# Performance work log

Measured on AMD Instinct MI355X. Metric: run time of the kernel, lower is better.

Reference implementation:

```python
import jax, jax.numpy as jnp
import numpy as np

NUM_STEPS = 151
STEP = 2.0 / (NUM_STEPS - 1)
TSIZE = NUM_STEPS  # t = -1, -1+step, ..., 1
N = 4096
D = 512
NUM_CLASSES = 100


def setup_inputs() -> dict:
    key = jax.random.key(0)
    k1, k2 = jax.random.split(key)
    feats = jax.random.normal(k1, (N, D), dtype=jnp.float32)
    # L2-normalize so pairwise dot products lie in [-1, 1] (histogram support)
    feats = feats / jnp.linalg.norm(feats, axis=1, keepdims=True)
    classes = jax.random.randint(k2, (N,), 0, NUM_CLASSES, dtype=jnp.int64)
    return {"features": feats, "classes": classes}


def reference(features, classes):
    n = features.shape[0]
    # pairwise cosine similarities, upper triangle (i < j)
    dists = features @ features.T  # [N, N]
    iu, ju = jnp.triu_indices(n, k=1)  # static index arrays
    s = dists[iu, ju]                  # [P] similarities
    pos = classes[iu] == classes[ju]   # [P] same-class mask

    # triangular soft-binning exactly as in the torch code:
    # f = floor(s/step)*step; bin at t==f gets (s-f)/step, bin at t==f+step gets (f+step-s)/step
    f = jnp.floor(s / STEP) * STEP
    j = jnp.floor(s / STEP).astype(jnp.int32) + (NUM_STEPS - 1) // 2  # index of t == f
    wa = (s - f) / STEP
    wb = (f + STEP - s) / STEP
    va = (j >= 0) & (j < TSIZE)
    vb = (j + 1 >= 0) & (j + 1 < TSIZE)
    ja = jnp.clip(j, 0, TSIZE - 1)
    jb = jnp.clip(j + 1, 0, TSIZE - 1)

    def hist(mask, size):
        w_a = jnp.where(va & mask, wa, 0.0)
        w_b = jnp.where(vb & mask, wb, 0.0)
        h = jnp.zeros(TSIZE, s.dtype).at[ja].add(w_a).at[jb].add(w_b)
        return h / size.astype(s.dtype)

    pos_size = pos.sum()
    neg_size = (~pos).sum()
    hist_pos = hist(pos, pos_size)
    hist_neg = hist(~pos, neg_size)
    # tril-masked repeat + sum(0) == inclusive cumulative sum of hist_pos
    hist_pos_cdf = jnp.cumsum(hist_pos)
    loss = jnp.sum(hist_neg * hist_pos_cdf)
    return loss
```

## Files before the change

### kernel.cpp

```cpp
#include <hip/hip_runtime.h>


#define N_PTS   4096
#define DIM     512
#define TSIZE   151
#define HALF_T  75
#define BM      128
#define BK      64
#define NSTEP   24
#define NTILES  32
#define NBLOCKS 528
#define P_TOTAL 8386560u
#define STEPF   (2.0f / 150.0f)
#define STEPINV 75.0f
#define NCOPY   8
#define HSTRIDE 309

typedef short bfrag __attribute__((ext_vector_type(8)));
typedef float ffrag __attribute__((ext_vector_type(4)));
typedef unsigned short u16;
typedef unsigned int   u32;

__device__ __forceinline__ ffrag mfma16(bfrag a, bfrag b, ffrag c) {
  return __builtin_amdgcn_mfma_f32_16x16x32_bf16(a, b, c, 0, 0, 0);
}

__device__ __forceinline__ void split4(float4 v, uint2* hi, uint2* lo) {
  u32 u0 = __float_as_uint(v.x), u1 = __float_as_uint(v.y);
  u32 u2 = __float_as_uint(v.z), u3 = __float_as_uint(v.w);
  float r0 = v.x - __uint_as_float(u0 & 0xFFFF0000u);
  float r1 = v.y - __uint_as_float(u1 & 0xFFFF0000u);
  float r2 = v.z - __uint_as_float(u2 & 0xFFFF0000u);
  float r3 = v.w - __uint_as_float(u3 & 0xFFFF0000u);
  hi->x = (u0 >> 16) | (u1 & 0xFFFF0000u);
  hi->y = (u2 >> 16) | (u3 & 0xFFFF0000u);
  lo->x = (__float_as_uint(r0) >> 16) | (__float_as_uint(r1) & 0xFFFF0000u);
  lo->y = (__float_as_uint(r2) >> 16) | (__float_as_uint(r3) & 0xFFFF0000u);
}

__device__ __forceinline__ void tile_decode(int orig, int* bi_, int* bj_) {
  int sbid = (orig & 7) * 66 + (orig >> 3);
  int rem = sbid, cnt = NTILES, bi = 0;
  while (rem >= cnt) { rem -= cnt; --cnt; ++bi; }
  *bi_ = bi; *bj_ = bi + rem;
}

__device__ __forceinline__ void stage_step(
    int s, u16* Ad, u16* Bd,
    const u16* __restrict__ Fhi, const u16* __restrict__ Flo,
    int rowA, int rowB, int w, int rseg, int swzk)
{
  const int region = s >> 3;
  const int k0 = (s & 7) * BK;
  const u16* ap = (region == 1) ? Flo : Fhi;
  const u16* bp = (region == 2) ? Flo : Fhi;
  #pragma unroll
  for (int g = 0; g < 4; ++g) {
    int seg = w * 4 + g;
    int row = seg * 8 + rseg;
    size_t ga = (size_t)(rowA + row) * DIM + k0 + swzk;
    size_t gb = (size_t)(rowB + row) * DIM + k0 + swzk;
    __builtin_amdgcn_global_load_lds(
        (const __attribute__((address_space(1))) unsigned int*)(ap + ga),
        (__attribute__((address_space(3))) unsigned int*)(Ad + seg * 512),
        16, 0, 0);
    __builtin_amdgcn_global_load_lds(
        (const __attribute__((address_space(1))) unsigned int*)(bp + gb),
        (__attribute__((address_space(3))) unsigned int*)(Bd + seg * 512),
        16, 0, 0);
  }
}

__device__ __forceinline__ void compute_step(
    const u16* As, const u16* Bs, ffrag (&acc)[4][4],
    int wy, int wx, int l4, int l16)
{
  const int swz = (l16 & 7) << 3;
  #pragma unroll
  for (int ks = 0; ks < 2; ++ks) {
    bfrag a[4], b[4];
    #pragma unroll
    for (int f = 0; f < 4; ++f) {
      int ra = wy * 64 + f * 16 + l16;
      int rb = wx * 64 + f * 16 + l16;
      int ko = (ks * 32 + l4 * 8) ^ swz;
      a[f] = *(const bfrag*)(As + ra * BK + ko);
      b[f] = *(const bfrag*)(Bs + rb * BK + ko);
    }
    #pragma unroll
    for (int fj = 0; fj < 4; ++fj)
      #pragma unroll
      for (int fi = 0; fi < 4; ++fi)
        acc[fi][fj] = mfma16(a[fi], b[fj], acc[fi][fj]);
  }
}

__device__ __forceinline__ void bin_epilogue(
    const ffrag (&acc)[4][4], float* h, const int* clsA, const int* clsB,
    int wy, int wx, int l4, int l16, bool diag, u32* myPos)
{
  #pragma unroll
  for (int fi = 0; fi < 4; ++fi) {
    #pragma unroll
    for (int fj = 0; fj < 4; ++fj) {
      #pragma unroll
      for (int r = 0; r < 4; ++r) {
        int li = wy * 64 + fi * 16 + l4 * 4 + r;
        int lj = wx * 64 + fj * 16 + l16;
        if (diag && li >= lj) continue;
        float s  = acc[fi][fj][r];
        float jf = floorf(s * STEPINV);
        int   jb = (int)jf + HALF_T;
        float f  = jf * STEPF;
        float wa = (s - f) * STEPINV;
        float wb = (f + STEPF - s) * STEPINV;
        bool  pos = (clsA[li] == clsB[lj]);
        *myPos += pos ? 1u : 0u;
        int off = pos ? 0 : TSIZE;
        if (jb >= 0 && jb < TSIZE)         unsafeAtomicAdd(h + off + jb, wa);
        if (jb + 1 >= 0 && jb + 1 < TSIZE) unsafeAtomicAdd(h + off + jb + 1, wb);
      }
    }
  }
}

__global__ __launch_bounds__(256) void presplit(
    const float* __restrict__ F, u16* __restrict__ Fhi, u16* __restrict__ Flo,
    float* __restrict__ g_hist, u32* __restrict__ g_pos)
{
  int u = blockIdx.x * 256 + threadIdx.x;
  int row = u >> 6, kb = u & 63;
  const float* src = F + (size_t)row * DIM + kb * 8;
  float4 v0 = *(const float4*)(src);
  float4 v1 = *(const float4*)(src + 4);
  uint2 h0, l0, h1, l1;
  split4(v0, &h0, &l0);
  split4(v1, &h1, &l1);
  uint4 hv; hv.x = h0.x; hv.y = h0.y; hv.z = h1.x; hv.w = h1.y;
  uint4 lv; lv.x = l0.x; lv.y = l0.y; lv.z = l1.x; lv.w = l1.y;
  size_t dst = (size_t)row * DIM + kb * 8;
  *(uint4*)(Fhi + dst) = hv;
  *(uint4*)(Flo + dst) = lv;
  if (blockIdx.x == 0) {
    for (int i = threadIdx.x; i < 2 * TSIZE; i += 256) g_hist[i] = 0.0f;
    if (threadIdx.x == 0) *g_pos = 0u;
  }
}

__global__ __launch_bounds__(256, 2) void hist_mfma(
    const u16* __restrict__ Fhi, const u16* __restrict__ Flo,
    const int* __restrict__ cls,
    float* __restrict__ g_hist, u32* __restrict__ g_pos)
{
  __shared__ __align__(16) u16 As0[BM * BK];
  __shared__ __align__(16) u16 As1[BM * BK];
  __shared__ __align__(16) u16 Bs0[BM * BK];
  __shared__ __align__(16) u16 Bs1[BM * BK];
  __shared__ float hist[NCOPY * HSTRIDE];
  __shared__ int clsA[BM], clsB[BM];
  __shared__ u32 posCount;

  const int t = threadIdx.x;
  int bi, bj;
  tile_decode((int)blockIdx.x, &bi, &bj);
  const int rowA = bi * BM, rowB = bj * BM;

  for (int i = t; i < NCOPY * HSTRIDE; i += 256) hist[i] = 0.0f;
  if (t < BM) clsA[t] = cls[rowA + t];
  else        clsB[t - BM] = cls[rowB + (t - BM)];
  if (t == 0) posCount = 0u;

  const int lane = t & 63, w = t >> 6;
  const int wy = w >> 1, wx = w & 1;
  const int l4 = lane >> 4, l16 = lane & 15;
  const int rseg = lane >> 3;
  const int swzk = ((lane & 7) ^ (lane >> 3)) << 3;

  ffrag acc[4][4] = {};

  stage_step(0, As0, Bs0, Fhi, Flo, rowA, rowB, w, rseg, swzk);
  __syncthreads();

  #pragma unroll 1
  for (int s2 = 0; s2 < NSTEP / 2; ++s2) {
    const int s = s2 * 2;
    if (s + 1 < NSTEP) stage_step(s + 1, As1, Bs1, Fhi, Flo, rowA, rowB, w, rseg, swzk);
    compute_step(As0, Bs0, acc, wy, wx, l4, l16);
    __syncthreads();
    if (s + 2 < NSTEP) stage_step(s + 2, As0, Bs0, Fhi, Flo, rowA, rowB, w, rseg, swzk);
    compute_step(As1, Bs1, acc, wy, wx, l4, l16);
    __syncthreads();
  }

  u32 myPos = 0;
  float* h = hist + (lane & 7) * HSTRIDE;
  bin_epilogue(acc, h, clsA, clsB, wy, wx, l4, l16, bi == bj, &myPos);
  atomicAdd(&posCount, myPos);
  __syncthreads();

  for (int i = t; i < 2 * TSIZE; i += 256) {
    float v = 0.0f;
    #pragma unroll
    for (int c = 0; c < NCOPY; ++c) v += hist[c * HSTRIDE + i];
    unsafeAtomicAdd(g_hist + i, v);
  }
  if (t == 0) atomicAdd(g_pos, posCount);
}

__global__ __launch_bounds__(256) void finalize(
    const float* __restrict__ g_hist,
    const u32* __restrict__ g_pos,
    float* __restrict__ out)
{
  __shared__ float hp[TSIZE];
  __shared__ float hn[TSIZE];
  __shared__ float red[4];
  const int t = threadIdx.x;
  const float Np = (float)(*g_pos);
  const float Nn = (float)(P_TOTAL - *g_pos);
  if (t < TSIZE) {
    hp[t] = g_hist[t] / Np;
    hn[t] = g_hist[TSIZE + t] / Nn;
  }
  __syncthreads();
  for (int off = 1; off < TSIZE; off <<= 1) {
    float v = 0.0f;
    if (t < TSIZE && t >= off) v = hp[t - off];
    __syncthreads();
    if (t < TSIZE) hp[t] += v;
    __syncthreads();
  }
  float term = (t < TSIZE) ? hn[t] * hp[t] : 0.0f;
  #pragma unroll
  for (int o = 32; o > 0; o >>= 1) term += __shfl_down(term, o);
  if ((t & 63) == 0) red[t >> 6] = term;
  __syncthreads();
  if (t == 0) *out = red[0] + red[1] + red[2] + red[3];
}

extern "C" void kernel_launch(void* const* d_in, const int* in_sizes, int n_in,
                              void* d_out, int out_size, void* d_ws, size_t ws_size,
                              hipStream_t stream) {
  const float* F   = (const float*)d_in[0];
  const int*   cls = (const int*)d_in[1];
  float* g_hist = (float*)d_ws;
  u32*   g_pos  = (u32*)((char*)d_ws + 2 * TSIZE * sizeof(float));
  float* out = (float*)d_out;

  const size_t offH = 65536;
  u16* Fhi = (u16*)((char*)d_ws + offH);
  u16* Flo = (u16*)((char*)d_ws + offH + (size_t)N_PTS * DIM * sizeof(u16));

  presplit<<<(N_PTS * 64) / 256, 256, 0, stream>>>(F, Fhi, Flo, g_hist, g_pos);
  hist_mfma<<<NBLOCKS, 256, 0, stream>>>(Fhi, Flo, cls, g_hist, g_pos);
  finalize<<<1, 256, 0, stream>>>(g_hist, g_pos, out);
}
```

Baseline: 234.5 us.

## Single-buffer LDS for 3 blocks/CU and XCD-aware band tile mapping

```diff
diff --git a/kernel.cpp b/kernel.cpp
--- a/kernel.cpp
+++ b/kernel.cpp
@@ -8,13 +8,12 @@
 #define BM      128
 #define BK      64
 #define NSTEP   24
-#define NTILES  32
-#define NBLOCKS 528
 #define P_TOTAL 8386560u
 #define STEPF   (2.0f / 150.0f)
 #define STEPINV 75.0f
 #define NCOPY   8
 #define HSTRIDE 309
+#define GRID    576
 
 typedef short bfrag __attribute__((ext_vector_type(8)));
 typedef float ffrag __attribute__((ext_vector_type(4)));
@@ -38,11 +37,24 @@
   lo->y = (__float_as_uint(r2) >> 16) | (__float_as_uint(r3) & 0xFFFF0000u);
 }
 
-__device__ __forceinline__ void tile_decode(int orig, int* bi_, int* bj_) {
-  int sbid = (orig & 7) * 66 + (orig >> 3);
-  int rem = sbid, cnt = NTILES, bi = 0;
-  while (rem >= cnt) { rem -= cnt; --cnt; ++bi; }
-  *bi_ = bi; *bj_ = bi + rem;
+__device__ __forceinline__ bool tile_decode(int bid, int* bi_, int* bj_) {
+  const int xcd = bid & 7, slot = bid >> 3;
+  if (xcd < 6) {
+    if (slot >= 64) return false;
+    const int BA[6] = {0, 0, 0, 1, 1, 2};
+    const int BB[6] = {1, 2, 3, 2, 3, 3};
+    *bi_ = BA[xcd] * 8 + (slot >> 3);
+    *bj_ = BB[xcd] * 8 + (slot & 7);
+  } else {
+    int p = slot;
+    int band = (xcd - 6) * 2 + (p >= 36 ? 1 : 0);
+    if (p >= 36) p -= 36;
+    int rem = p, cnt = 8, ii = 0;
+    while (rem >= cnt) { rem -= cnt; --cnt; ++ii; }
+    *bi_ = band * 8 + ii;
+    *bj_ = band * 8 + ii + rem;
+  }
+  return true;
 }
 
 __device__ __forceinline__ void stage_step(
@@ -147,22 +159,20 @@
   }
 }
 
-__global__ __launch_bounds__(256, 2) void hist_mfma(
+__global__ __launch_bounds__(256, 3) void hist_mfma(
     const u16* __restrict__ Fhi, const u16* __restrict__ Flo,
     const int* __restrict__ cls,
     float* __restrict__ g_hist, u32* __restrict__ g_pos)
 {
-  __shared__ __align__(16) u16 As0[BM * BK];
-  __shared__ __align__(16) u16 As1[BM * BK];
-  __shared__ __align__(16) u16 Bs0[BM * BK];
-  __shared__ __align__(16) u16 Bs1[BM * BK];
+  __shared__ __align__(16) u16 As[BM * BK];
+  __shared__ __align__(16) u16 Bs[BM * BK];
   __shared__ float hist[NCOPY * HSTRIDE];
   __shared__ int clsA[BM], clsB[BM];
   __shared__ u32 posCount;
 
+  int bi, bj;
+  if (!tile_decode((int)blockIdx.x, &bi, &bj)) return;
   const int t = threadIdx.x;
-  int bi, bj;
-  tile_decode((int)blockIdx.x, &bi, &bj);
   const int rowA = bi * BM, rowB = bj * BM;
 
   for (int i = t; i < NCOPY * HSTRIDE; i += 256) hist[i] = 0.0f;
@@ -178,18 +188,12 @@
 
   ffrag acc[4][4] = {};
 
-  stage_step(0, As0, Bs0, Fhi, Flo, rowA, rowB, w, rseg, swzk);
-  __syncthreads();
-
   #pragma unroll 1
-  for (int s2 = 0; s2 < NSTEP / 2; ++s2) {
-    const int s = s2 * 2;
-    if (s + 1 < NSTEP) stage_step(s + 1, As1, Bs1, Fhi, Flo, rowA, rowB, w, rseg, swzk);
-    compute_step(As0, Bs0, acc, wy, wx, l4, l16);
-    __syncthreads();
-    if (s + 2 < NSTEP) stage_step(s + 2, As0, Bs0, Fhi, Flo, rowA, rowB, w, rseg, swzk);
-    compute_step(As1, Bs1, acc, wy, wx, l4, l16);
-    __syncthreads();
+  for (int s = 0; s < NSTEP; ++s) {
+    __syncthreads();
+    stage_step(s, As, Bs, Fhi, Flo, rowA, rowB, w, rseg, swzk);
+    __syncthreads();
+    compute_step(As, Bs, acc, wy, wx, l4, l16);
   }
 
   u32 myPos = 0;
@@ -252,6 +256,6 @@
   u16* Flo = (u16*)((char*)d_ws + offH + (size_t)N_PTS * DIM * sizeof(u16));
 
   presplit<<<(N_PTS * 64) / 256, 256, 0, stream>>>(F, Fhi, Flo, g_hist, g_pos);
-  hist_mfma<<<NBLOCKS, 256, 0, stream>>>(Fhi, Flo, cls, g_hist, g_pos);
+  hist_mfma<<<GRID, 256, 0, stream>>>(Fhi, Flo, cls, g_hist, g_pos);
   finalize<<<1, 256, 0, stream>>>(g_hist, g_pos, out);
 }
```

Result: faster. 219.9 us (-6.2%).
